# Kernel optimization log

Measured on AMD Instinct MI355X. Metric: run time of the kernel, lower is better.

## Reference

```python
import jax, jax.numpy as jnp
import numpy as np

# Static config (must match init_kwargs)
IMG_H, IMG_W = 48, 160
BEV_H, BEV_W = 128, 128
X_MIN, X_MAX, Y_MIN, Y_MAX = -51.2, 51.2, -51.2, 51.2
RES_X = (X_MAX - X_MIN) / BEV_W
RES_Y = (Y_MAX - Y_MIN) / BEV_H
C, D, B = 128, 64, 2


def setup_inputs() -> dict:
    key = jax.random.key(0)
    k1, k2, k3, k4 = jax.random.split(key, 4)
    img_features = jax.random.normal(k1, (B, C, IMG_H, IMG_W), dtype=jnp.float32)
    # depth distribution per pixel (softmax over D, as a depth net would emit)
    depth_probs = jax.nn.softmax(jax.random.normal(k2, (B, D, IMG_H, IMG_W), dtype=jnp.float32), axis=1)
    # depth bin centers: 1m .. 60m
    depth_values = jnp.linspace(1.0, 60.0, D, dtype=jnp.float32)
    # realistic pinhole intrinsics (feature-map scale) with tiny per-cam jitter
    fx, fy, cx, cy = 120.0, 120.0, IMG_W / 2.0, IMG_H / 2.0
    K0 = jnp.array([[fx, 0.0, cx], [0.0, fy, cy], [0.0, 0.0, 1.0]], dtype=jnp.float32)
    K = K0[None] + 0.01 * jax.random.normal(k3, (B, 3, 3), dtype=jnp.float32) * jnp.array(
        [[1.0, 0.0, 1.0], [0.0, 1.0, 1.0], [0.0, 0.0, 0.0]], dtype=jnp.float32)
    # cam->lidar extrinsic: cam z (forward) -> lidar x, cam x -> -lidar y, cam y -> -lidar z
    R0 = jnp.array([[0.0, 0.0, 1.0], [-1.0, 0.0, 0.0], [0.0, -1.0, 0.0]], dtype=jnp.float32)
    t0 = jnp.array([1.5, 0.0, 1.8], dtype=jnp.float32)
    T0 = jnp.eye(4, dtype=jnp.float32).at[:3, :3].set(R0).at[:3, 3].set(t0)
    T = T0[None] + jnp.zeros((B, 4, 4), dtype=jnp.float32)
    T = T.at[:, :3, 3].add(0.05 * jax.random.normal(k4, (B, 3), dtype=jnp.float32))
    return {"img_features": img_features, "depth_probs": depth_probs,
            "depth_values": depth_values, "K": K, "T": T}


def _lss_forward(img_features, depth_probs, depth_values, K, T):
    Bn, Cn, H, W = img_features.shape
    Dn = depth_values.shape[0]
    # homogeneous pixel grid [H, W, 3]
    gx, gy = jnp.meshgrid(jnp.arange(W, dtype=jnp.float32),
                          jnp.arange(H, dtype=jnp.float32), indexing="xy")
    grid = jnp.stack([gx, gy, jnp.ones_like(gx)], axis=-1)
    # unproject: rays [B, H, W, 3]
    K_inv = jnp.linalg.inv(K)
    rays = jnp.einsum("bij,hwj->bhwi", K_inv, grid)
    # points in camera frame [B, D, H, W, 3]
    pts_cam = depth_values[None, :, None, None, None] * rays[:, None]
    # camera -> lidar
    pts = jnp.einsum("bij,bdhwj->bdhwi", T[:, :3, :3], pts_cam) + T[:, None, None, None, :3, 3]
    x, y, z = pts[..., 0], pts[..., 1], pts[..., 2]
    # torch .long() truncates toward zero -> astype int32 matches
    bx = ((x - X_MIN) / RES_X).astype(jnp.int32)
    by = ((y - Y_MIN) / RES_Y).astype(jnp.int32)
    valid = (bx >= 0) & (bx < BEV_W) & (by >= 0) & (by < BEV_H) & (z > 0)
    # depth-weighted features [B, D, H, W, C], masked instead of gathered
    weighted = jnp.einsum("bchw,bdhw->bdhwc", img_features, depth_probs)
    weighted = weighted * valid[..., None]
    idx = jnp.where(valid, by * BEV_W + bx, 0).reshape(Bn, -1)
    feats = weighted.reshape(Bn, -1, Cn)
    bev_flat = jax.vmap(lambda f, i: jax.ops.segment_sum(f, i, num_segments=BEV_H * BEV_W))(feats, idx)
    return bev_flat.reshape(Bn, BEV_H, BEV_W, Cn).transpose(0, 3, 1, 2)


def reference(img_features, depth_probs, depth_values, K, T):
    return _lss_forward(img_features, depth_probs, depth_values, K, T)
```

## Files before the change

### kernel.cpp

```cpp
#include <hip/hip_runtime.h>

constexpr int IMG_H = 48, IMG_W = 160;
constexpr int HW    = IMG_H * IMG_W;
constexpr int BEV_H = 128, BEV_W = 128;
constexpr int NCELL = BEV_H * BEV_W;
constexpr int C_DIM = 128, D_DIM = 64, B_DIM = 2;
constexpr int NCELL_TOT = B_DIM * NCELL;
constexpr int NPIX_TOT  = B_DIM * HW;
constexpr int NPTS      = NPIX_TOT * D_DIM;
constexpr int MAX_ENTRIES = NPTS;
constexpr int CHUNK = 64;
constexpr int WAVES_PER_BLK = 4;
constexpr int NSHARD = 16;
constexpr int CNT_BLOCKS = NPTS / 256;
constexpr int TRN_BLOCKS = (HW / 32) * (C_DIM / 32) * B_DIM;
constexpr int SCAN_BLOCKS = NCELL_TOT / 256;
constexpr float X_MIN = -51.2f, Y_MIN = -51.2f;
constexpr float RES_X = 102.4f / 128.0f;
constexpr float RES_Y = 102.4f / 128.0f;

typedef _Float16 half2v __attribute__((ext_vector_type(2)));

constexpr size_t WS_IMG_T = 0;
constexpr size_t WS_FLAGS = WS_IMG_T + (size_t)B_DIM * HW * C_DIM / 2;
constexpr size_t WS_HIST2 = WS_FLAGS + 128;
constexpr size_t WS_OUT_T = WS_HIST2 + (size_t)NSHARD * NCELL_TOT;
constexpr size_t WS_OFFS  = WS_OUT_T + (size_t)NCELL_TOT * C_DIM;
constexpr size_t WS_EKEY  = WS_OFFS + NCELL_TOT + 4;
constexpr size_t WS_EW16  = WS_EKEY + MAX_ENTRIES;
constexpr size_t MEMSET_WORDS = 128 + (size_t)NSHARD * NCELL_TOT + (size_t)NCELL_TOT * C_DIM;

__device__ inline int point_shard(int tid) {
    return ((tid >> 2) + (tid >> 8)) & (NSHARD - 1);
}

__device__ inline void make_ray(const float* __restrict__ K, int b, float gx, float gy,
                                float& rx, float& ry, float& rz) {
    const float* Kb = K + b * 9;
    const float a00 = Kb[0], a01 = Kb[1], a02 = Kb[2];
    const float a10 = Kb[3], a11 = Kb[4], a12 = Kb[5];
    const float a20 = Kb[6], a21 = Kb[7], a22 = Kb[8];
    const float det = a00 * (a11 * a22 - a12 * a21)
                    - a01 * (a10 * a22 - a12 * a20)
                    + a02 * (a10 * a21 - a11 * a20);
    const float inv = 1.0f / det;
    const float i00 =  (a11 * a22 - a12 * a21) * inv;
    const float i01 = -(a01 * a22 - a02 * a21) * inv;
    const float i02 =  (a01 * a12 - a02 * a11) * inv;
    const float i10 = -(a10 * a22 - a12 * a20) * inv;
    const float i11 =  (a00 * a22 - a02 * a20) * inv;
    const float i12 = -(a00 * a12 - a02 * a10) * inv;
    const float i20 =  (a10 * a21 - a11 * a20) * inv;
    const float i21 = -(a00 * a21 - a01 * a20) * inv;
    const float i22 =  (a00 * a11 - a01 * a10) * inv;
    rx = i00 * gx + i01 * gy + i02;
    ry = i10 * gx + i11 * gy + i12;
    rz = i20 * gx + i21 * gy + i22;
}

__device__ inline int point_gcell(int tid, const float* __restrict__ dv,
                                  const float* __restrict__ K,
                                  const float* __restrict__ T) {
    const int pix = tid % HW;
    const int bd  = tid / HW;
    const int d   = bd % D_DIM;
    const int b   = bd / D_DIM;
    const int h = pix / IMG_W, w = pix % IMG_W;
    float rx, ry, rz;
    make_ray(K, b, (float)w, (float)h, rx, ry, rz);
    const float* Tb = T + b * 16;
    const float dep = dv[d];
    const float px = dep * rx, py = dep * ry, pz = dep * rz;
    const float x = Tb[0] * px + Tb[1] * py + Tb[2]  * pz + Tb[3];
    const float y = Tb[4] * px + Tb[5] * py + Tb[6]  * pz + Tb[7];
    const float z = Tb[8] * px + Tb[9] * py + Tb[10] * pz + Tb[11];
    const int bx = (int)((x - X_MIN) / RES_X);
    const int by = (int)((y - Y_MIN) / RES_Y);
    const bool valid = (bx >= 0) && (bx < BEV_W) && (by >= 0) && (by < BEV_H) && (z > 0.0f);
    return valid ? (b * NCELL + by * BEV_W + bx) : -1;
}

__device__ inline bool wave_runs(int gcell, int lane, int& run_len, int& leader_idx) {
    const int left = __shfl_up(gcell, 1);
    const bool is_leader = (lane == 0) || (left != gcell);
    const unsigned long long lmask = __ballot(is_leader);
    const unsigned long long rest = (lane == 63) ? 0ULL : (lmask >> (lane + 1));
    const int f = __ffsll((unsigned long long)rest);
    run_len = f ? f : (64 - lane);
    const unsigned long long below =
        lmask & ((lane == 63) ? ~0ULL : ((1ULL << (lane + 1)) - 1ULL));
    leader_idx = 63 - __clzll((long long)below);
    return is_leader;
}

__global__ __launch_bounds__(256) void k_prep(const float* __restrict__ img,
                                              _Float16* __restrict__ img_t,
                                              const float* __restrict__ dv,
                                              const float* __restrict__ K,
                                              const float* __restrict__ T,
                                              int* __restrict__ hist2) {
    __shared__ float tile[32][33];
    if (blockIdx.x < CNT_BLOCKS) {
        const int tid = blockIdx.x * 256 + threadIdx.x;
        const int gcell = point_gcell(tid, dv, K, T);
        const int lane = threadIdx.x & 63;
        int run_len, leader_idx;
        const bool lead = wave_runs(gcell, lane, run_len, leader_idx);
        if (lead && gcell >= 0)
            atomicAdd(&hist2[(size_t)point_shard(tid) * NCELL_TOT + gcell], run_len);
    } else {
        const int bi = blockIdx.x - CNT_BLOCKS;
        const int px_t = bi % (HW / 32);
        const int c_t  = (bi / (HW / 32)) % (C_DIM / 32);
        const int b    = bi / ((HW / 32) * (C_DIM / 32));
        const int tx = threadIdx.x & 31, ty = threadIdx.x >> 5;
        const int pix0 = px_t * 32, c0 = c_t * 32;
        #pragma unroll
        for (int j = 0; j < 32; j += 8)
            tile[ty + j][tx] = img[((size_t)(b * C_DIM + c0 + ty + j)) * HW + pix0 + tx];
        __syncthreads();
        #pragma unroll
        for (int j = 0; j < 32; j += 8)
            img_t[((size_t)(b * HW + pix0 + ty + j)) * C_DIM + c0 + tx] =
                (_Float16)tile[tx][ty + j];
    }
}

__global__ __launch_bounds__(256) void k_scan_fused(int* __restrict__ hist2,
                                                    int* __restrict__ offs,
                                                    unsigned* __restrict__ flags) {
    __shared__ int lds[256];
    __shared__ int s_base;
    const int b = blockIdx.x;
    const int t = threadIdx.x;
    const int cell = b * 256 + t;
    int run = 0;
    #pragma unroll
    for (int sh = 0; sh < NSHARD; ++sh) {
        const size_t idx = (size_t)sh * NCELL_TOT + cell;
        const int c = hist2[idx];
        hist2[idx] = run;
        run += c;
    }
    const int h = run;
    lds[t] = h;
    __syncthreads();
    #pragma unroll
    for (int off = 1; off < 256; off <<= 1) {
        const int v = (t >= off) ? lds[t - off] : 0;
        __syncthreads();
        lds[t] += v;
        __syncthreads();
    }
    const int incl = lds[t];
    const int S = lds[255];
    if (t == 0) {
        const unsigned w = (((b == 0) ? 2u : 1u) << 30) | (unsigned)S;
        __hip_atomic_store(&flags[b], w, __ATOMIC_RELEASE, __HIP_MEMORY_SCOPE_AGENT);
        if (b == 0) s_base = 0;
    }
    if (b > 0 && t < 64) {
        int sum = 0;
        int p = b - 1;
        bool done = false;
        while (!done) {
            const int idx = p - t;
            unsigned w;
            if (idx >= 0) {
                do {
                    w = __hip_atomic_load(&flags[idx], __ATOMIC_ACQUIRE,
                                          __HIP_MEMORY_SCOPE_AGENT);
                } while ((w >> 30) == 0);
            } else {
                w = 2u << 30;
            }
            const unsigned long long m2 = __ballot((w >> 30) == 2u);
            const int first2 = __ffsll(m2) - 1;
            const int limit = (first2 < 0) ? 63 : first2;
            int contrib = (t <= limit && idx >= 0) ? (int)(w & 0x3FFFFFFFu) : 0;
            #pragma unroll
            for (int o = 32; o > 0; o >>= 1) contrib += __shfl_down(contrib, o);
            sum += __shfl(contrib, 0);
            if (first2 >= 0) done = true;
            else p -= 64;
        }
        if (t == 0) {
            s_base = sum;
            const unsigned w2 = (2u << 30) | (unsigned)(sum + S);
            __hip_atomic_store(&flags[b], w2, __ATOMIC_RELEASE, __HIP_MEMORY_SCOPE_AGENT);
        }
    }
    __syncthreads();
    const int base = s_base;
    offs[cell] = base + incl - h;
    if (cell == NCELL_TOT - 1) offs[NCELL_TOT] = base + S;
}

__global__ __launch_bounds__(256) void k_fill(const float* __restrict__ dp,
                                              const float* __restrict__ dv,
                                              const float* __restrict__ K,
                                              const float* __restrict__ T,
                                              const int* __restrict__ offs,
                                              int* __restrict__ cursor2,
                                              int* __restrict__ ekey,
                                              unsigned short* __restrict__ ew16) {
    const int tid = blockIdx.x * 256 + threadIdx.x;
    const int gcell = point_gcell(tid, dv, K, T);
    const int lane = threadIdx.x & 63;
    int run_len, leader_idx;
    const bool lead = wave_runs(gcell, lane, run_len, leader_idx);
    int base = 0;
    if (lead && gcell >= 0)
        base = offs[gcell]
             + atomicAdd(&cursor2[(size_t)point_shard(tid) * NCELL_TOT + gcell], run_len);
    base = __shfl(base, leader_idx);
    if (gcell < 0) return;
    const int slot = base + (lane - leader_idx);
    const float p = dp[tid];
    ekey[slot] = (gcell << 13) | (tid % HW);
    ew16[slot] = (unsigned short)__float2uint_rn(p * 65535.0f);
}

__global__ __launch_bounds__(256) void k_chunk_gather(
    const _Float16* __restrict__ img_t,
    const int* __restrict__ offs,
    const int* __restrict__ ekey,
    const unsigned short* __restrict__ ew16,
    float* __restrict__ out_t)
{
    const int total = offs[NCELL_TOT];
    const int wave  = threadIdx.x >> 6;
    const int lane  = threadIdx.x & 63;
    const int base  = (blockIdx.x * WAVES_PER_BLK + wave) * CHUNK;
    if (base >= total) return;

    const int eidx = min(base + lane, total - 1);
    const int   mykey = ekey[eidx];
    const float myw   = (base + lane < total)
                        ? (float)ew16[base + lane] * (1.0f / 65535.0f) : 0.0f;
    const int mywi = __float_as_int(myw);

    const int c2 = lane * 2;
    const int fc    = __builtin_amdgcn_readlane(mykey, 0) >> 13;
    const int lcell = __builtin_amdgcn_readlane(mykey, 63) >> 13;
    const bool shared_first = (base > 0) && ((ekey[base - 1] >> 13) == fc);
    const bool shared_last  = (base + CHUNK < total) && ((ekey[base + CHUNK] >> 13) == lcell);

    int prev = fc;
    float2 acc = make_float2(0.0f, 0.0f);

#define LOADG(g, V)                                                              \
    do {                                                                         \
        _Pragma("unroll")                                                        \
        for (int k = 0; k < 8; ++k) {                                            \
            const int key = __builtin_amdgcn_readlane(mykey, (g) * 8 + k);       \
            const int pix = key & 8191;                                          \
            const int bb  = key >> 27;                                           \
            V[k] = *reinterpret_cast<const half2v*>(                             \
                &img_t[((size_t)(bb * HW + pix)) * C_DIM + c2]);                 \
        }                                                                        \
    } while (0)

#define FLUSHP(cell)                                                             \
    do {                                                                         \
        float* o = &out_t[(size_t)(cell) * C_DIM + c2];                          \
        const bool shared_ = ((cell) == fc && shared_first) ||                   \
                             ((cell) == lcell && shared_last);                   \
        if (shared_) {                                                           \
            atomicAdd(o, acc.x);                                                 \
            atomicAdd(o + 1, acc.y);                                             \
        } else {                                                                 \
            *reinterpret_cast<float2*>(o) = acc;            \
        }                                                                        \
    } while (0)

#define ACCG(g, V)                                                               \
    do {                                                                         \
        _Pragma("unroll")                                                        \
        for (int k = 0; k < 8; ++k) {                                            \
            const int   key = __builtin_amdgcn_readlane(mykey, (g) * 8 + k);     \
            const float wgt =                                                    \
                __int_as_float(__builtin_amdgcn_readlane(mywi, (g) * 8 + k));    \
            const int gcell = key >> 13;                                         \
            if (gcell != prev) {                              \
                FLUSHP(prev);                                                    \
                acc = make_float2(0.0f, 0.0f);                                   \
                prev = gcell;                                                    \
            }                                                                    \
            acc.x = fmaf((float)V[k][0], wgt, acc.x);                            \
            acc.y = fmaf((float)V[k][1], wgt, acc.y);                            \
        }                                                                        \
    } while (0)

    half2v va[8], vb[8];
    LOADG(0, va);
    LOADG(1, vb);
    ACCG(0, va);
    LOADG(2, va);
    ACCG(1, vb);
    LOADG(3, vb);
    ACCG(2, va);
    LOADG(4, va);
    ACCG(3, vb);
    LOADG(5, vb);
    ACCG(4, va);
    LOADG(6, va);
    ACCG(5, vb);
    LOADG(7, vb);
    ACCG(6, va);
    ACCG(7, vb);
    FLUSHP(prev);

#undef LOADG
#undef FLUSHP
#undef ACCG
}

__global__ __launch_bounds__(256) void k_untranspose(const float* __restrict__ out_t,
                                                     float* __restrict__ out) {
    __shared__ float tile[32][33];
    const int b = blockIdx.z;
    const int tx = threadIdx.x, ty = threadIdx.y;
    const int cell0 = blockIdx.x * 32, c0 = blockIdx.y * 32;
    const float* src = out_t + (size_t)b * NCELL * C_DIM;
    #pragma unroll
    for (int j = 0; j < 32; j += 8)
        tile[ty + j][tx] = src[((size_t)(cell0 + ty + j)) * C_DIM + c0 + tx];
    __syncthreads();
    #pragma unroll
    for (int j = 0; j < 32; j += 8)
        out[((size_t)(b * C_DIM + c0 + ty + j)) * NCELL + cell0 + tx] = tile[tx][ty + j];
}

extern "C" void kernel_launch(void* const* d_in, const int* in_sizes, int n_in,
                              void* d_out, int out_size, void* d_ws, size_t ws_size,
                              hipStream_t stream) {
    const float* img = (const float*)d_in[0];
    const float* dp  = (const float*)d_in[1];
    const float* dv  = (const float*)d_in[2];
    const float* K   = (const float*)d_in[3];
    const float* T   = (const float*)d_in[4];
    float* out = (float*)d_out;

    _Float16* img_t = (_Float16*)d_ws;
    unsigned* flags = (unsigned*)((int*)d_ws + WS_FLAGS);
    int*   hist2  = (int*)d_ws + WS_HIST2;
    float* out_t  = (float*)d_ws + WS_OUT_T;
    int*   offs   = (int*)d_ws + WS_OFFS;
    int*   ekey   = (int*)d_ws + WS_EKEY;
    unsigned short* ew16 = (unsigned short*)((int*)d_ws + WS_EW16);
    (void)ws_size;

    hipMemsetAsync(flags, 0, MEMSET_WORDS * sizeof(int), stream);

    k_prep<<<CNT_BLOCKS + TRN_BLOCKS, 256, 0, stream>>>(img, img_t, dv, K, T, hist2);
    k_scan_fused<<<SCAN_BLOCKS, 256, 0, stream>>>(hist2, offs, flags);
    k_fill<<<NPTS / 256, 256, 0, stream>>>(dp, dv, K, T, offs, hist2, ekey, ew16);
    constexpr int GATHER_BLOCKS = MAX_ENTRIES / (CHUNK * WAVES_PER_BLK);
    k_chunk_gather<<<GATHER_BLOCKS, 256, 0, stream>>>(img_t, offs, ekey, ew16, out_t);
    k_untranspose<<<dim3(NCELL / 32, C_DIM / 32, B_DIM), dim3(32, 8), 0, stream>>>(
        out_t, out);
}
```

Before: 140.7 us.

## Fuse scan into prep kernel via last-blocks roles and zero out_t in-kernel

Merges the histogram scan kernel into the prep kernel. A global done counter hands the last 128 finishing blocks the scan roles, and each waits until every prep block has finished before running the decoupled-lookback scan. The 16 MB out_t buffer is now zeroed by the prep threads instead of hipMemsetAsync, which removes one launch and one large memset. The cost is spin-waiting blocks and the reliance on blocks being co-resident to avoid deadlock.

```diff
diff --git a/kernel.cpp b/kernel.cpp
--- a/kernel.cpp
+++ b/kernel.cpp
@@ -14,7 +14,8 @@
 constexpr int NSHARD = 16;
 constexpr int CNT_BLOCKS = NPTS / 256;
 constexpr int TRN_BLOCKS = (HW / 32) * (C_DIM / 32) * B_DIM;
-constexpr int SCAN_BLOCKS = NCELL_TOT / 256;
+constexpr int PREP_TOTAL = CNT_BLOCKS + TRN_BLOCKS;
+constexpr int SCAN_ROLES = 128;
 constexpr float X_MIN = -51.2f, Y_MIN = -51.2f;
 constexpr float RES_X = 102.4f / 128.0f;
 constexpr float RES_Y = 102.4f / 128.0f;
@@ -22,13 +23,15 @@
 typedef _Float16 half2v __attribute__((ext_vector_type(2)));
 
 constexpr size_t WS_IMG_T = 0;
-constexpr size_t WS_FLAGS = WS_IMG_T + (size_t)B_DIM * HW * C_DIM / 2;
+constexpr size_t WS_DONE  = WS_IMG_T + (size_t)B_DIM * HW * C_DIM / 2;
+constexpr size_t WS_FLAGS = WS_DONE + 4;
 constexpr size_t WS_HIST2 = WS_FLAGS + 128;
 constexpr size_t WS_OUT_T = WS_HIST2 + (size_t)NSHARD * NCELL_TOT;
 constexpr size_t WS_OFFS  = WS_OUT_T + (size_t)NCELL_TOT * C_DIM;
 constexpr size_t WS_EKEY  = WS_OFFS + NCELL_TOT + 4;
 constexpr size_t WS_EW16  = WS_EKEY + MAX_ENTRIES;
-constexpr size_t MEMSET_WORDS = 128 + (size_t)NSHARD * NCELL_TOT + (size_t)NCELL_TOT * C_DIM;
+constexpr size_t MEMSET_WORDS = 4 + 128 + (size_t)NSHARD * NCELL_TOT;
+constexpr int OUT_T_F4 = NCELL_TOT * C_DIM / 4;
 
 __device__ inline int point_shard(int tid) {
     return ((tid >> 2) + (tid >> 8)) & (NSHARD - 1);
@@ -98,12 +101,26 @@
                                               const float* __restrict__ dv,
                                               const float* __restrict__ K,
                                               const float* __restrict__ T,
-                                              int* __restrict__ hist2) {
+                                              int* __restrict__ hist2,
+                                              float4* __restrict__ out_t4,
+                                              int* __restrict__ done,
+                                              unsigned* __restrict__ flags,
+                                              int* __restrict__ offs) {
     __shared__ float tile[32][33];
+    __shared__ int lds[256];
+    __shared__ int s_role;
+    __shared__ int s_base;
+    const int t = threadIdx.x;
+
+    {
+        const int i = blockIdx.x * 256 + t;
+        if (i < OUT_T_F4) out_t4[i] = make_float4(0.f, 0.f, 0.f, 0.f);
+    }
+
     if (blockIdx.x < CNT_BLOCKS) {
-        const int tid = blockIdx.x * 256 + threadIdx.x;
+        const int tid = blockIdx.x * 256 + t;
         const int gcell = point_gcell(tid, dv, K, T);
-        const int lane = threadIdx.x & 63;
+        const int lane = t & 63;
         int run_len, leader_idx;
         const bool lead = wave_runs(gcell, lane, run_len, leader_idx);
         if (lead && gcell >= 0)
@@ -113,7 +130,7 @@
         const int px_t = bi % (HW / 32);
         const int c_t  = (bi / (HW / 32)) % (C_DIM / 32);
         const int b    = bi / ((HW / 32) * (C_DIM / 32));
-        const int tx = threadIdx.x & 31, ty = threadIdx.x >> 5;
+        const int tx = t & 31, ty = t >> 5;
         const int pix0 = px_t * 32, c0 = c_t * 32;
         #pragma unroll
         for (int j = 0; j < 32; j += 8)
@@ -124,21 +141,28 @@
             img_t[((size_t)(b * HW + pix0 + ty + j)) * C_DIM + c0 + tx] =
                 (_Float16)tile[tx][ty + j];
     }
-}
-
-__global__ __launch_bounds__(256) void k_scan_fused(int* __restrict__ hist2,
-                                                    int* __restrict__ offs,
-                                                    unsigned* __restrict__ flags) {
-    __shared__ int lds[256];
-    __shared__ int s_base;
-    const int b = blockIdx.x;
-    const int t = threadIdx.x;
-    const int cell = b * 256 + t;
+
+    if (t == 0) {
+        const int tk = __hip_atomic_fetch_add(done, 1, __ATOMIC_ACQ_REL,
+                                              __HIP_MEMORY_SCOPE_AGENT);
+        s_role = tk - (PREP_TOTAL - SCAN_ROLES);
+        if (s_role >= 0) {
+            while (__hip_atomic_load(done, __ATOMIC_ACQUIRE,
+                                     __HIP_MEMORY_SCOPE_AGENT) < PREP_TOTAL)
+                __builtin_amdgcn_s_sleep(1);
+        }
+    }
+    __syncthreads();
+    const int role = s_role;
+    if (role < 0) return;
+
+    const int cell = role * 256 + t;
     int run = 0;
     #pragma unroll
     for (int sh = 0; sh < NSHARD; ++sh) {
         const size_t idx = (size_t)sh * NCELL_TOT + cell;
-        const int c = hist2[idx];
+        const int c = __hip_atomic_load(&hist2[idx], __ATOMIC_RELAXED,
+                                        __HIP_MEMORY_SCOPE_AGENT);
         hist2[idx] = run;
         run += c;
     }
@@ -155,15 +179,15 @@
     const int incl = lds[t];
     const int S = lds[255];
     if (t == 0) {
-        const unsigned w = (((b == 0) ? 2u : 1u) << 30) | (unsigned)S;
-        __hip_atomic_store(&flags[b], w, __ATOMIC_RELEASE, __HIP_MEMORY_SCOPE_AGENT);
-        if (b == 0) s_base = 0;
-    }
-    if (b > 0 && t < 64) {
+        const unsigned w = (((role == 0) ? 2u : 1u) << 30) | (unsigned)S;
+        __hip_atomic_store(&flags[role], w, __ATOMIC_RELEASE, __HIP_MEMORY_SCOPE_AGENT);
+        if (role == 0) s_base = 0;
+    }
+    if (role > 0 && t < 64) {
         int sum = 0;
-        int p = b - 1;
-        bool done = false;
-        while (!done) {
+        int p = role - 1;
+        bool done2 = false;
+        while (!done2) {
             const int idx = p - t;
             unsigned w;
             if (idx >= 0) {
@@ -181,13 +205,13 @@
             #pragma unroll
             for (int o = 32; o > 0; o >>= 1) contrib += __shfl_down(contrib, o);
             sum += __shfl(contrib, 0);
-            if (first2 >= 0) done = true;
+            if (first2 >= 0) done2 = true;
             else p -= 64;
         }
         if (t == 0) {
             s_base = sum;
             const unsigned w2 = (2u << 30) | (unsigned)(sum + S);
-            __hip_atomic_store(&flags[b], w2, __ATOMIC_RELEASE, __HIP_MEMORY_SCOPE_AGENT);
+            __hip_atomic_store(&flags[role], w2, __ATOMIC_RELEASE, __HIP_MEMORY_SCOPE_AGENT);
         }
     }
     __syncthreads();
@@ -343,6 +367,7 @@
     float* out = (float*)d_out;
 
     _Float16* img_t = (_Float16*)d_ws;
+    int*   done   = (int*)d_ws + WS_DONE;
     unsigned* flags = (unsigned*)((int*)d_ws + WS_FLAGS);
     int*   hist2  = (int*)d_ws + WS_HIST2;
     float* out_t  = (float*)d_ws + WS_OUT_T;
@@ -351,10 +376,10 @@
     unsigned short* ew16 = (unsigned short*)((int*)d_ws + WS_EW16);
     (void)ws_size;
 
-    hipMemsetAsync(flags, 0, MEMSET_WORDS * sizeof(int), stream);
-
-    k_prep<<<CNT_BLOCKS + TRN_BLOCKS, 256, 0, stream>>>(img, img_t, dv, K, T, hist2);
-    k_scan_fused<<<SCAN_BLOCKS, 256, 0, stream>>>(hist2, offs, flags);
+    hipMemsetAsync(done, 0, MEMSET_WORDS * sizeof(int), stream);
+
+    k_prep<<<PREP_TOTAL, 256, 0, stream>>>(img, img_t, dv, K, T, hist2,
+                                           (float4*)out_t, done, flags, offs);
     k_fill<<<NPTS / 256, 256, 0, stream>>>(dp, dv, K, T, offs, hist2, ekey, ew16);
     constexpr int GATHER_BLOCKS = MAX_ENTRIES / (CHUNK * WAVES_PER_BLK);
     k_chunk_gather<<<GATHER_BLOCKS, 256, 0, stream>>>(img_t, offs, ekey, ew16, out_t);
```

Result: slower. 328.0 us (+133.1%).

## Zero accumulation buffer inside prep kernel and replace lookback scan with atomic bases

Applied to the files above, without the earlier changes.

The zeroing of the transposed output accumulator moves out of the host memset and into the k_prep kernel, each thread writing one float4 of zeros. This shrinks the memset to only the totals and histogram shards and drops one large separate pass over memory. The decoupled-lookback prefix scan is replaced by each block taking its base offset with an atomicAdd on a global total. Block bases are then assigned in arrival order, not in block order, so cell segments are no longer laid out in ascending cell order. Any consumer that assumes the segment for the last cell of a block ends at the next cell's offset could be affected.

```diff
diff --git a/kernel.cpp b/kernel.cpp
--- a/kernel.cpp
+++ b/kernel.cpp
@@ -14,6 +14,7 @@
 constexpr int NSHARD = 16;
 constexpr int CNT_BLOCKS = NPTS / 256;
 constexpr int TRN_BLOCKS = (HW / 32) * (C_DIM / 32) * B_DIM;
+constexpr int PREP_TOTAL = CNT_BLOCKS + TRN_BLOCKS;
 constexpr int SCAN_BLOCKS = NCELL_TOT / 256;
 constexpr float X_MIN = -51.2f, Y_MIN = -51.2f;
 constexpr float RES_X = 102.4f / 128.0f;
@@ -22,13 +23,14 @@
 typedef _Float16 half2v __attribute__((ext_vector_type(2)));
 
 constexpr size_t WS_IMG_T = 0;
-constexpr size_t WS_FLAGS = WS_IMG_T + (size_t)B_DIM * HW * C_DIM / 2;
-constexpr size_t WS_HIST2 = WS_FLAGS + 128;
+constexpr size_t WS_TOT   = WS_IMG_T + (size_t)B_DIM * HW * C_DIM / 2;
+constexpr size_t WS_HIST2 = WS_TOT + 4;
 constexpr size_t WS_OUT_T = WS_HIST2 + (size_t)NSHARD * NCELL_TOT;
 constexpr size_t WS_OFFS  = WS_OUT_T + (size_t)NCELL_TOT * C_DIM;
 constexpr size_t WS_EKEY  = WS_OFFS + NCELL_TOT + 4;
 constexpr size_t WS_EW16  = WS_EKEY + MAX_ENTRIES;
-constexpr size_t MEMSET_WORDS = 128 + (size_t)NSHARD * NCELL_TOT + (size_t)NCELL_TOT * C_DIM;
+constexpr size_t MEMSET_WORDS = 4 + (size_t)NSHARD * NCELL_TOT;
+constexpr int OUT_T_F4 = NCELL_TOT * C_DIM / 4;
 
 __device__ inline int point_shard(int tid) {
     return ((tid >> 2) + (tid >> 8)) & (NSHARD - 1);
@@ -98,12 +100,20 @@
                                               const float* __restrict__ dv,
                                               const float* __restrict__ K,
                                               const float* __restrict__ T,
-                                              int* __restrict__ hist2) {
+                                              int* __restrict__ hist2,
+                                              float4* __restrict__ out_t4) {
     __shared__ float tile[32][33];
+    const int t = threadIdx.x;
+
+    {
+        const int i = blockIdx.x * 256 + t;
+        if (i < OUT_T_F4) out_t4[i] = make_float4(0.f, 0.f, 0.f, 0.f);
+    }
+
     if (blockIdx.x < CNT_BLOCKS) {
-        const int tid = blockIdx.x * 256 + threadIdx.x;
+        const int tid = blockIdx.x * 256 + t;
         const int gcell = point_gcell(tid, dv, K, T);
-        const int lane = threadIdx.x & 63;
+        const int lane = t & 63;
         int run_len, leader_idx;
         const bool lead = wave_runs(gcell, lane, run_len, leader_idx);
         if (lead && gcell >= 0)
@@ -113,7 +123,7 @@
         const int px_t = bi % (HW / 32);
         const int c_t  = (bi / (HW / 32)) % (C_DIM / 32);
         const int b    = bi / ((HW / 32) * (C_DIM / 32));
-        const int tx = threadIdx.x & 31, ty = threadIdx.x >> 5;
+        const int tx = t & 31, ty = t >> 5;
         const int pix0 = px_t * 32, c0 = c_t * 32;
         #pragma unroll
         for (int j = 0; j < 32; j += 8)
@@ -126,9 +136,9 @@
     }
 }
 
-__global__ __launch_bounds__(256) void k_scan_fused(int* __restrict__ hist2,
-                                                    int* __restrict__ offs,
-                                                    unsigned* __restrict__ flags) {
+__global__ __launch_bounds__(256) void k_scan(int* __restrict__ hist2,
+                                              int* __restrict__ offs,
+                                              int* __restrict__ tot) {
     __shared__ int lds[256];
     __shared__ int s_base;
     const int b = blockIdx.x;
@@ -155,45 +165,13 @@
     const int incl = lds[t];
     const int S = lds[255];
     if (t == 0) {
-        const unsigned w = (((b == 0) ? 2u : 1u) << 30) | (unsigned)S;
-        __hip_atomic_store(&flags[b], w, __ATOMIC_RELEASE, __HIP_MEMORY_SCOPE_AGENT);
-        if (b == 0) s_base = 0;
-    }
-    if (b > 0 && t < 64) {
-        int sum = 0;
-        int p = b - 1;
-        bool done = false;
-        while (!done) {
-            const int idx = p - t;
-            unsigned w;
-            if (idx >= 0) {
-                do {
-                    w = __hip_atomic_load(&flags[idx], __ATOMIC_ACQUIRE,
-                                          __HIP_MEMORY_SCOPE_AGENT);
-                } while ((w >> 30) == 0);
-            } else {
-                w = 2u << 30;
-            }
-            const unsigned long long m2 = __ballot((w >> 30) == 2u);
-            const int first2 = __ffsll(m2) - 1;
-            const int limit = (first2 < 0) ? 63 : first2;
-            int contrib = (t <= limit && idx >= 0) ? (int)(w & 0x3FFFFFFFu) : 0;
-            #pragma unroll
-            for (int o = 32; o > 0; o >>= 1) contrib += __shfl_down(contrib, o);
-            sum += __shfl(contrib, 0);
-            if (first2 >= 0) done = true;
-            else p -= 64;
-        }
-        if (t == 0) {
-            s_base = sum;
-            const unsigned w2 = (2u << 30) | (unsigned)(sum + S);
-            __hip_atomic_store(&flags[b], w2, __ATOMIC_RELEASE, __HIP_MEMORY_SCOPE_AGENT);
-        }
+        s_base = atomicAdd(&tot[0], S);
+        const int arr = atomicAdd(&tot[1], 1);
+        if (arr == SCAN_BLOCKS - 1)
+            offs[NCELL_TOT] = atomicAdd(&tot[0], 0);
     }
     __syncthreads();
-    const int base = s_base;
-    offs[cell] = base + incl - h;
-    if (cell == NCELL_TOT - 1) offs[NCELL_TOT] = base + S;
+    offs[cell] = s_base + incl - h;
 }
 
 __global__ __launch_bounds__(256) void k_fill(const float* __restrict__ dp,
@@ -343,7 +321,7 @@
     float* out = (float*)d_out;
 
     _Float16* img_t = (_Float16*)d_ws;
-    unsigned* flags = (unsigned*)((int*)d_ws + WS_FLAGS);
+    int*   tot    = (int*)d_ws + WS_TOT;
     int*   hist2  = (int*)d_ws + WS_HIST2;
     float* out_t  = (float*)d_ws + WS_OUT_T;
     int*   offs   = (int*)d_ws + WS_OFFS;
@@ -351,10 +329,11 @@
     unsigned short* ew16 = (unsigned short*)((int*)d_ws + WS_EW16);
     (void)ws_size;
 
-    hipMemsetAsync(flags, 0, MEMSET_WORDS * sizeof(int), stream);
-
-    k_prep<<<CNT_BLOCKS + TRN_BLOCKS, 256, 0, stream>>>(img, img_t, dv, K, T, hist2);
-    k_scan_fused<<<SCAN_BLOCKS, 256, 0, stream>>>(hist2, offs, flags);
+    hipMemsetAsync(tot, 0, MEMSET_WORDS * sizeof(int), stream);
+
+    k_prep<<<PREP_TOTAL, 256, 0, stream>>>(img, img_t, dv, K, T, hist2,
+                                           (float4*)out_t);
+    k_scan<<<SCAN_BLOCKS, 256, 0, stream>>>(hist2, offs, tot);
     k_fill<<<NPTS / 256, 256, 0, stream>>>(dp, dv, K, T, offs, hist2, ekey, ew16);
     constexpr int GATHER_BLOCKS = MAX_ENTRIES / (CHUNK * WAVES_PER_BLK);
     k_chunk_gather<<<GATHER_BLOCKS, 256, 0, stream>>>(img_t, offs, ekey, ew16, out_t);
```

Result: no change. 141.0 us (+0.2%).
